# Performance work log

Hardware: AMD Instinct MI355X
Metric: run time of the kernel (lower is better)

## Reference

```python
import jax, jax.numpy as jnp
import numpy as np

N_USER = 100000
N_ITEM = 50000
N = N_USER + N_ITEM  # 150000 nodes
D = 64               # embedding_size
L = 3                # num_layers
E = 2000000          # edges
B = 8192             # batch of (user, item_p, item_n) triples
INT_W, POP_W, TIDE_W = 0.1, 0.1, 0.2


def setup_inputs() -> dict:
    key = jax.random.key(0)
    ks = jax.random.split(key, 10)
    stdv = 1.0 / np.sqrt(D)
    emb_int = jax.random.uniform(ks[0], (N, D), minval=-stdv, maxval=stdv, dtype=jnp.float32)
    emb_pop = jax.random.uniform(ks[1], (N, D), minval=-stdv, maxval=stdv, dtype=jnp.float32)
    q = jax.random.uniform(ks[2], (N_ITEM,), dtype=jnp.float32)
    b = jax.random.uniform(ks[3], (N_ITEM,), dtype=jnp.float32)
    user = jax.random.randint(ks[4], (B, 1), 0, N_USER)
    item_p = jax.random.randint(ks[5], (B, 1), 0, N_ITEM)
    item_n = jax.random.randint(ks[6], (B, 1), 0, N_ITEM)
    mask = jax.random.randint(ks[7], (B, 1), 0, 2).astype(bool)
    edge_src = jax.random.randint(ks[8], (E,), 0, N)
    edge_dst = jax.random.randint(ks[9], (E,), 0, N)
    return {"emb_int": emb_int, "emb_pop": emb_pop, "q": q, "b": b,
            "user": user, "item_p": item_p, "item_n": item_n, "mask": mask,
            "edge_src": edge_src, "edge_dst": edge_dst}


def reference(emb_int, emb_pop, q, b, user, item_p, item_n, mask, edge_src, edge_dst):
    # --- LightGCN symmetric normalization coefficients (per edge) ---
    ones = jnp.ones(edge_src.shape, emb_int.dtype)
    deg_out = jax.ops.segment_sum(ones, edge_src, num_segments=N)
    deg_in = jax.ops.segment_sum(ones, edge_dst, num_segments=N)
    norm = (jax.lax.rsqrt(jnp.maximum(deg_out, 1.0))[edge_src]
            * jax.lax.rsqrt(jnp.maximum(deg_in, 1.0))[edge_dst])  # [E]

    def propagate(e0):
        # L layers of LGConv (gather-scale-scatter), mean over layer outputs incl. layer 0.
        # Dropout is identity in eval mode (training=False).
        acc, h = e0, e0
        for _ in range(L):
            h = jax.ops.segment_sum(h[edge_src] * norm[:, None], edge_dst, num_segments=N)
            acc = acc + h
        return acc / (L + 1)

    f_int = propagate(emb_int)  # [N, D]
    f_pop = propagate(emb_pop)  # [N, D]

    ip = item_p + N_USER  # item node ids
    inn = item_n + N_USER
    u_i, u_p = f_int[user], f_pop[user]          # [B, 1, D]
    pi_i, pi_p = f_int[ip], f_pop[ip]
    ni_i, ni_p = f_int[inn], f_pop[inn]

    p_score_int = jnp.sum(u_i * pi_i, axis=2)    # [B, 1]
    n_score_int = jnp.sum(u_i * ni_i, axis=2)
    p_score_pop = jnp.sum(u_p * pi_p, axis=2)
    n_score_pop = jnp.sum(u_p * ni_p, axis=2)
    p_score_total = p_score_int + p_score_pop
    n_score_total = n_score_int + n_score_pop

    mf = mask.astype(p_score_int.dtype)
    nmf = (~mask).astype(p_score_int.dtype)

    def mask_bpr(p, n, m):
        return -jnp.mean(m * jax.nn.log_sigmoid(p - n))

    def bpr(p, n):
        return -jnp.mean(jax.nn.log_sigmoid(p - n))

    loss_int = mask_bpr(p_score_int, n_score_int, mf)
    loss_pop = mask_bpr(n_score_pop, p_score_pop, mf) - mask_bpr(p_score_pop, n_score_pop, nmf)

    pop_p = jax.nn.softplus(q[item_p]) + jax.nn.softplus(b[item_p])  # [B, 1]
    pop_n = jax.nn.softplus(q[item_n]) + jax.nn.softplus(b[item_n])
    loss_tide = bpr(jnp.tanh(pop_p) * p_score_total, jnp.tanh(pop_n) * n_score_total)

    return INT_W * loss_int + POP_W * loss_pop + TIDE_W * loss_tide
```

## Files before the change

### kernel.cpp

```cpp
#include <hip/hip_runtime.h>
#include <hip/hip_bf16.h>
#include <math.h>

#define N_USER 100000
#define N_ITEM 50000
#define NNODE  150000
#define DIM    64
#define NEDGE  2000000
#define BSZ    8192
#define NTGT   (3*BSZ)
#define CB     586
#define NB     512
#define CH     ((NEDGE + NB - 1)/NB)
#define LBLK   2048
#define PREPB  (NNODE*32/256)
#define CAP    5120

typedef float v2f __attribute__((ext_vector_type(2)));

__device__ __forceinline__ float logsigf(float x){
    return fminf(x, 0.f) - log1pf(expf(-fabsf(x)));
}
__device__ __forceinline__ float softplusf(float x){
    return fmaxf(x, 0.f) + log1pf(expf(-fabsf(x)));
}
__device__ __forceinline__ v2f fp8x2_to_f32(unsigned short u){
    return __builtin_amdgcn_cvt_pk_f32_fp8((int)u, false);
}
__device__ __forceinline__ unsigned short f32_to_fp8x2(float a, float b){
    return (unsigned short)__builtin_amdgcn_cvt_pk_fp8_f32(a, b, 0, false);
}
__device__ __forceinline__ unsigned rfl(unsigned v){
    return (unsigned)__builtin_amdgcn_readfirstlane((int)v);
}

__device__ __forceinline__ void scanCB(unsigned* arr, unsigned* tmp){
    int t = threadIdx.x;
    int base = 3*t;
    unsigned a0=0,a1=0,a2=0;
    if(base   < CB) a0 = arr[base];
    if(base+1 < CB) a1 = arr[base+1];
    if(base+2 < CB) a2 = arr[base+2];
    unsigned s = a0+a1+a2;
    tmp[t]=s; __syncthreads();
    for(int off=1; off<256; off<<=1){
        unsigned v = (t>=off)? tmp[t-off] : 0u;
        __syncthreads();
        tmp[t] += v;
        __syncthreads();
    }
    unsigned excl = tmp[t]-s;
    if(base   < CB) arr[base]   = excl;
    if(base+1 < CB) arr[base+1] = excl+a0;
    if(base+2 < CB) arr[base+2] = excl+a0+a1;
    __syncthreads();
}

__global__ __launch_bounds__(256) void k_hist(const int* __restrict__ src, const int* __restrict__ dst,
                       unsigned* __restrict__ histD, unsigned* __restrict__ histS,
                       const float2* __restrict__ ei, const float2* __restrict__ ep,
                       unsigned* __restrict__ hC32,
                       const unsigned char* __restrict__ mask8, unsigned* __restrict__ mflag){
    if(blockIdx.x >= NB){
        if(blockIdx.x == NB + PREPB){
            __shared__ int any;
            if(threadIdx.x==0) any=0;
            __syncthreads();
            for(int i=threadIdx.x;i<BSZ;i+=256){ if((i&3) && mask8[i]) any=1; }
            __syncthreads();
            if(threadIdx.x==0) *mflag = (any!=0) ? 1u : 0u;
            return;
        }
        int idx = (blockIdx.x - NB)*256 + threadIdx.x;
        int n = idx>>5, c = idx&31;
        float2 va, vb;
        if(c<16){ va = ei[(size_t)n*32 + 2*c]; vb = ei[(size_t)n*32 + 2*c+1]; }
        else    { va = ep[(size_t)n*32 + 2*c-32]; vb = ep[(size_t)n*32 + 2*c-31]; }
        int d = __builtin_amdgcn_cvt_pk_fp8_f32(va.x, va.y, 0, false);
        d = __builtin_amdgcn_cvt_pk_fp8_f32(vb.x, vb.y, d, true);
        hC32[(size_t)n*32 + c] = (unsigned)d;
        return;
    }
    __shared__ unsigned hD[CB], hS[CB];
    for(int i=threadIdx.x;i<CB;i+=256){ hD[i]=0; hS[i]=0; }
    __syncthreads();
    int lo = blockIdx.x*CH, hi = min(lo+CH, NEDGE);
    for(int e=lo+threadIdx.x; e<hi; e+=256){
        atomicAdd(&hS[src[e]>>8],1u);
        atomicAdd(&hD[dst[e]>>8],1u);
    }
    __syncthreads();
    for(int i=threadIdx.x;i<CB;i+=256){
        histD[(size_t)i*NB + blockIdx.x]=hD[i];
        histS[(size_t)i*NB + blockIdx.x]=hS[i];
    }
}

__global__ __launch_bounds__(512) void k_colscan(unsigned* __restrict__ histD, unsigned* __restrict__ histS,
                          unsigned* __restrict__ ctD, unsigned* __restrict__ ctS){
    unsigned* hist = blockIdx.y ? histS : histD;
    unsigned* ct   = blockIdx.y ? ctS   : ctD;
    int b = blockIdx.x;
    __shared__ unsigned sh[512];
    unsigned v = hist[(size_t)b*NB + threadIdx.x];
    sh[threadIdx.x] = v;
    __syncthreads();
    for(int off=1; off<512; off<<=1){
        unsigned t = (threadIdx.x>=off)? sh[threadIdx.x-off] : 0u;
        __syncthreads();
        sh[threadIdx.x] += t;
        __syncthreads();
    }
    hist[(size_t)b*NB + threadIdx.x] = sh[threadIdx.x] - v;
    if(threadIdx.x==511) ct[b] = sh[511];
}

__global__ __launch_bounds__(1024) void k_bstart(const unsigned* __restrict__ ctD, const unsigned* __restrict__ ctS,
                         unsigned* __restrict__ bsD, unsigned* __restrict__ bsS){
    __shared__ unsigned sh[1024];
    unsigned v = (threadIdx.x<CB)? ctD[threadIdx.x] : 0u;
    sh[threadIdx.x]=v; __syncthreads();
    for(int off=1; off<1024; off<<=1){ unsigned t=(threadIdx.x>=off)?sh[threadIdx.x-off]:0u; __syncthreads(); sh[threadIdx.x]+=t; __syncthreads(); }
    if(threadIdx.x<CB) bsD[threadIdx.x]=sh[threadIdx.x]-v;
    if(threadIdx.x==CB-1) bsD[CB]=sh[threadIdx.x];
    __syncthreads();
    unsigned v2 = (threadIdx.x<CB)? ctS[threadIdx.x] : 0u;
    sh[threadIdx.x]=v2; __syncthreads();
    for(int off=1; off<1024; off<<=1){ unsigned t=(threadIdx.x>=off)?sh[threadIdx.x-off]:0u; __syncthreads(); sh[threadIdx.x]+=t; __syncthreads(); }
    if(threadIdx.x<CB) bsS[threadIdx.x]=sh[threadIdx.x]-v2;
    if(threadIdx.x==CB-1) bsS[CB]=sh[threadIdx.x];
}

__global__ __launch_bounds__(256) void k_scatter(const int* __restrict__ src, const int* __restrict__ dst,
                          const unsigned* __restrict__ histD, const unsigned* __restrict__ histS,
                          const unsigned* __restrict__ bsD, const unsigned* __restrict__ bsS,
                          unsigned* __restrict__ part, unsigned char* __restrict__ spart){
    __shared__ unsigned curD[CB], curS[CB];
    __shared__ unsigned lhD[CB], lhS[CB];
    __shared__ unsigned startD[CB], startS[CB];
    __shared__ unsigned tmp[256];
    __shared__ unsigned partl[CH];
    __shared__ unsigned short keyD[CH];
    __shared__ unsigned short keyS[CH];
    __shared__ unsigned char sl[CH];
    for(int i=threadIdx.x;i<CB;i+=256){
        curD[i]=bsD[i]+histD[(size_t)i*NB+blockIdx.x];
        curS[i]=bsS[i]+histS[(size_t)i*NB+blockIdx.x];
        lhD[i]=0; lhS[i]=0;
    }
    __syncthreads();
    int lo=blockIdx.x*CH, hi=min(lo+CH,NEDGE);
    int n = hi-lo;
    for(int e=lo+threadIdx.x;e<hi;e+=256){
        atomicAdd(&lhD[dst[e]>>8],1u);
        atomicAdd(&lhS[src[e]>>8],1u);
    }
    __syncthreads();
    scanCB(lhD, tmp);
    scanCB(lhS, tmp);
    for(int i=threadIdx.x;i<CB;i+=256){ startD[i]=lhD[i]; startS[i]=lhS[i]; }
    __syncthreads();
    for(int e=lo+threadIdx.x;e<hi;e+=256){
        int s=src[e], d=dst[e];
        unsigned bd=(unsigned)(d>>8);
        unsigned slot=atomicAdd(&lhD[bd],1u);
        partl[slot]=((unsigned)(d&255)<<18)|(unsigned)s;
        keyD[slot]=(unsigned short)bd;
        unsigned bs=(unsigned)(s>>8);
        unsigned sslot=atomicAdd(&lhS[bs],1u);
        sl[sslot]=(unsigned char)(s&255);
        keyS[sslot]=(unsigned short)bs;
    }
    __syncthreads();
    for(int k=threadIdx.x;k<n;k+=256){
        unsigned b=keyD[k];
        part[curD[b] + (unsigned)k - startD[b]] = partl[k];
    }
    for(int k=threadIdx.x;k<n;k+=256){
        unsigned b=keyS[k];
        spart[curS[b] + (unsigned)k - startS[b]] = sl[k];
    }
}

__global__ __launch_bounds__(256) void k_degO(const unsigned char* __restrict__ spart, const unsigned* __restrict__ bsS,
                       float* __restrict__ rsqO){
    __shared__ unsigned cnt[256];
    cnt[threadIdx.x]=0;
    __syncthreads();
    unsigned lo=bsS[blockIdx.x], hi=bsS[blockIdx.x+1];
    for(unsigned e=lo+threadIdx.x;e<hi;e+=256) atomicAdd(&cnt[spart[e]],1u);
    __syncthreads();
    int node=(blockIdx.x<<8)+(int)threadIdx.x;
    if(node<NNODE) rsqO[node]=rsqrtf(fmaxf((float)cnt[threadIdx.x],1.f));
}

__global__ __launch_bounds__(256) void k_csr(const unsigned* __restrict__ part, const unsigned* __restrict__ bsD,
                      const float* __restrict__ rsqO,
                      unsigned* __restrict__ rs, unsigned* __restrict__ degI,
                      unsigned* __restrict__ ec){
    __shared__ unsigned cnt[256], cur[256], sh[256];
    __shared__ float rsq[256];
    __shared__ unsigned partl[CAP];
    cnt[threadIdx.x]=0;
    __syncthreads();
    unsigned lo=bsD[blockIdx.x], hi=bsD[blockIdx.x+1];
    unsigned n = hi-lo;
    for(unsigned e=lo+threadIdx.x;e<hi;e+=256) atomicAdd(&cnt[part[e]>>18],1u);
    __syncthreads();
    unsigned c=cnt[threadIdx.x];
    sh[threadIdx.x]=c; __syncthreads();
    for(int o=1;o<256;o<<=1){ unsigned t=(threadIdx.x>=o)?sh[threadIdx.x-o]:0u; __syncthreads(); sh[threadIdx.x]+=t; __syncthreads(); }
    unsigned ex = sh[threadIdx.x]-c;
    rsq[threadIdx.x]=rsqrtf(fmaxf((float)c,1.f));
    cur[threadIdx.x]=ex;
    int node=(blockIdx.x<<8)+(int)threadIdx.x;
    if(node<NNODE){ degI[node]=c; rs[node]=lo+ex; }
    __syncthreads();
    if(n <= CAP){
        for(unsigned e=lo+threadIdx.x;e<hi;e+=256){
            unsigned p=part[e];
            unsigned slot=atomicAdd(&cur[p>>18],1u);
            partl[slot]=p;
        }
        __syncthreads();
        for(unsigned k=threadIdx.x;k<n;k+=256){
            unsigned p=partl[k];
            unsigned fb=p>>18, s=p&0x3FFFFu;
            float w=rsq[fb]*rsqO[s];
            unsigned w14=(unsigned)(w*16383.f + 0.5f);
            ec[lo+k]=(w14<<18)|s;
        }
    } else {
        for(unsigned e=lo+threadIdx.x;e<hi;e+=256){
            unsigned p=part[e];
            unsigned fb=p>>18, s=p&0x3FFFFu;
            unsigned pos=lo+atomicAdd(&cur[fb],1u);
            float w=rsq[fb]*rsqO[s];
            unsigned w14=(unsigned)(w*16383.f + 0.5f);
            ec[pos]=(w14<<18)|s;
        }
    }
}

__device__ __forceinline__ void drain_row(const unsigned short* __restrict__ hin,
                                          const unsigned* __restrict__ ec,
                                          unsigned s, unsigned c, unsigned &i, int lane,
                                          float &ax, float &ay){
    for(; i+4<=c; i+=4){
        unsigned e0=ec[s+i], e1=ec[s+i+1], e2=ec[s+i+2], e3=ec[s+i+3];
        unsigned short u0=hin[(size_t)(e0&0x3FFFFu)*64+lane];
        unsigned short u1=hin[(size_t)(e1&0x3FFFFu)*64+lane];
        unsigned short u2=hin[(size_t)(e2&0x3FFFFu)*64+lane];
        unsigned short u3=hin[(size_t)(e3&0x3FFFFu)*64+lane];
        float w0=(float)(e0>>18)*(1.f/16383.f), w1=(float)(e1>>18)*(1.f/16383.f);
        float w2=(float)(e2>>18)*(1.f/16383.f), w3=(float)(e3>>18)*(1.f/16383.f);
        v2f v;
        v=fp8x2_to_f32(u0); ax+=w0*v.x; ay+=w0*v.y;
        v=fp8x2_to_f32(u1); ax+=w1*v.x; ay+=w1*v.y;
        v=fp8x2_to_f32(u2); ax+=w2*v.x; ay+=w2*v.y;
        v=fp8x2_to_f32(u3); ax+=w3*v.x; ay+=w3*v.y;
    }
    for(; i<c; ++i){
        unsigned e0=ec[s+i];
        unsigned short u0=hin[(size_t)(e0&0x3FFFFu)*64+lane];
        float w0=(float)(e0>>18)*(1.f/16383.f);
        v2f v=fp8x2_to_f32(u0); ax+=w0*v.x; ay+=w0*v.y;
    }
}

__global__ __launch_bounds__(256) void k_spmm_c(const unsigned short* __restrict__ hin, unsigned short* __restrict__ hout,
                                                const unsigned* __restrict__ rs, const unsigned* __restrict__ degI,
                                                const unsigned* __restrict__ ec){
    int wv = (blockIdx.x*256 + threadIdx.x) >> 6;
    int lane = threadIdx.x & 63;
    int r = 4*wv;
    if(r >= NNODE) return;
    unsigned s0=rfl(rs[r  ]), c0=rfl(degI[r  ]);
    unsigned s1=rfl(rs[r+1]), c1=rfl(degI[r+1]);
    unsigned s2=rfl(rs[r+2]), c2=rfl(degI[r+2]);
    unsigned s3=rfl(rs[r+3]), c3=rfl(degI[r+3]);
    float ax0=0,ay0=0, ax1=0,ay1=0, ax2=0,ay2=0, ax3=0,ay3=0;
    unsigned i0=0,i1=0,i2=0,i3=0;
    while(i0+4<=c0 && i1+4<=c1 && i2+4<=c2 && i3+4<=c3){
        unsigned e00=ec[s0+i0], e01=ec[s0+i0+1], e02=ec[s0+i0+2], e03=ec[s0+i0+3];
        unsigned e10=ec[s1+i1], e11=ec[s1+i1+1], e12=ec[s1+i1+2], e13=ec[s1+i1+3];
        unsigned e20=ec[s2+i2], e21=ec[s2+i2+1], e22=ec[s2+i2+2], e23=ec[s2+i2+3];
        unsigned e30=ec[s3+i3], e31=ec[s3+i3+1], e32=ec[s3+i3+2], e33=ec[s3+i3+3];
        unsigned short u00=hin[(size_t)(e00&0x3FFFFu)*64+lane];
        unsigned short u01=hin[(size_t)(e01&0x3FFFFu)*64+lane];
        unsigned short u02=hin[(size_t)(e02&0x3FFFFu)*64+lane];
        unsigned short u03=hin[(size_t)(e03&0x3FFFFu)*64+lane];
        unsigned short u10=hin[(size_t)(e10&0x3FFFFu)*64+lane];
        unsigned short u11=hin[(size_t)(e11&0x3FFFFu)*64+lane];
        unsigned short u12=hin[(size_t)(e12&0x3FFFFu)*64+lane];
        unsigned short u13=hin[(size_t)(e13&0x3FFFFu)*64+lane];
        unsigned short u20=hin[(size_t)(e20&0x3FFFFu)*64+lane];
        unsigned short u21=hin[(size_t)(e21&0x3FFFFu)*64+lane];
        unsigned short u22=hin[(size_t)(e22&0x3FFFFu)*64+lane];
        unsigned short u23=hin[(size_t)(e23&0x3FFFFu)*64+lane];
        unsigned short u30=hin[(size_t)(e30&0x3FFFFu)*64+lane];
        unsigned short u31=hin[(size_t)(e31&0x3FFFFu)*64+lane];
        unsigned short u32v=hin[(size_t)(e32&0x3FFFFu)*64+lane];
        unsigned short u33=hin[(size_t)(e33&0x3FFFFu)*64+lane];
        v2f v;
        v=fp8x2_to_f32(u00); ax0+=(float)(e00>>18)*(1.f/16383.f)*v.x; ay0+=(float)(e00>>18)*(1.f/16383.f)*v.y;
        v=fp8x2_to_f32(u01); ax0+=(float)(e01>>18)*(1.f/16383.f)*v.x; ay0+=(float)(e01>>18)*(1.f/16383.f)*v.y;
        v=fp8x2_to_f32(u02); ax0+=(float)(e02>>18)*(1.f/16383.f)*v.x; ay0+=(float)(e02>>18)*(1.f/16383.f)*v.y;
        v=fp8x2_to_f32(u03); ax0+=(float)(e03>>18)*(1.f/16383.f)*v.x; ay0+=(float)(e03>>18)*(1.f/16383.f)*v.y;
        v=fp8x2_to_f32(u10); ax1+=(float)(e10>>18)*(1.f/16383.f)*v.x; ay1+=(float)(e10>>18)*(1.f/16383.f)*v.y;
        v=fp8x2_to_f32(u11); ax1+=(float)(e11>>18)*(1.f/16383.f)*v.x; ay1+=(float)(e11>>18)*(1.f/16383.f)*v.y;
        v=fp8x2_to_f32(u12); ax1+=(float)(e12>>18)*(1.f/16383.f)*v.x; ay1+=(float)(e12>>18)*(1.f/16383.f)*v.y;
        v=fp8x2_to_f32(u13); ax1+=(float)(e13>>18)*(1.f/16383.f)*v.x; ay1+=(float)(e13>>18)*(1.f/16383.f)*v.y;
        v=fp8x2_to_f32(u20); ax2+=(float)(e20>>18)*(1.f/16383.f)*v.x; ay2+=(float)(e20>>18)*(1.f/16383.f)*v.y;
        v=fp8x2_to_f32(u21); ax2+=(float)(e21>>18)*(1.f/16383.f)*v.x; ay2+=(float)(e21>>18)*(1.f/16383.f)*v.y;
        v=fp8x2_to_f32(u22); ax2+=(float)(e22>>18)*(1.f/16383.f)*v.x; ay2+=(float)(e22>>18)*(1.f/16383.f)*v.y;
        v=fp8x2_to_f32(u23); ax2+=(float)(e23>>18)*(1.f/16383.f)*v.x; ay2+=(float)(e23>>18)*(1.f/16383.f)*v.y;
        v=fp8x2_to_f32(u30); ax3+=(float)(e30>>18)*(1.f/16383.f)*v.x; ay3+=(float)(e30>>18)*(1.f/16383.f)*v.y;
        v=fp8x2_to_f32(u31); ax3+=(float)(e31>>18)*(1.f/16383.f)*v.x; ay3+=(float)(e31>>18)*(1.f/16383.f)*v.y;
        v=fp8x2_to_f32(u32v); ax3+=(float)(e32>>18)*(1.f/16383.f)*v.x; ay3+=(float)(e32>>18)*(1.f/16383.f)*v.y;
        v=fp8x2_to_f32(u33); ax3+=(float)(e33>>18)*(1.f/16383.f)*v.x; ay3+=(float)(e33>>18)*(1.f/16383.f)*v.y;
        i0+=4; i1+=4; i2+=4; i3+=4;
    }
    drain_row(hin, ec, s0, c0, i0, lane, ax0, ay0);
    drain_row(hin, ec, s1, c1, i1, lane, ax1, ay1);
    drain_row(hin, ec, s2, c2, i2, lane, ax2, ay2);
    drain_row(hin, ec, s3, c3, i3, lane, ax3, ay3);
    hout[(size_t)(r  )*64+lane] = f32_to_fp8x2(ax0, ay0);
    hout[(size_t)(r+1)*64+lane] = f32_to_fp8x2(ax1, ay1);
    hout[(size_t)(r+2)*64+lane] = f32_to_fp8x2(ax2, ay2);
    hout[(size_t)(r+3)*64+lane] = f32_to_fp8x2(ax3, ay3);
}

__global__ __launch_bounds__(256) void k_spmm_t(const unsigned short* __restrict__ hin, float2* __restrict__ h3,
                                                const unsigned* __restrict__ rs, const unsigned* __restrict__ degI,
                                                const unsigned* __restrict__ ec,
                                                const int* __restrict__ user, const int* __restrict__ itp,
                                                const int* __restrict__ itn){
    int wv = (blockIdx.x*256 + threadIdx.x) >> 6;
    int lane = threadIdx.x & 63;
    int t0 = 2*wv, t1 = 2*wv+1;
    if(t0 >= NTGT) return;
    int sec0 = t0>>13, b0 = t0&(BSZ-1);
    int sec1 = t1>>13, b1 = t1&(BSZ-1);
    int n0 = (sec0==0) ? user[b0] : ((sec0==1) ? itp[b0]+N_USER : itn[b0]+N_USER);
    int n1 = (sec1==0) ? user[b1] : ((sec1==1) ? itp[b1]+N_USER : itn[b1]+N_USER);
    n0 = __builtin_amdgcn_readfirstlane(n0);
    n1 = __builtin_amdgcn_readfirstlane(n1);
    unsigned s0 = rfl(rs[n0]), c0 = rfl(degI[n0]);
    unsigned s1 = rfl(rs[n1]), c1 = rfl(degI[n1]);
    float ax0=0.f, ay0=0.f, ax1=0.f, ay1=0.f;
    unsigned i0=0, i1=0;
    while(i0+4<=c0 && i1+4<=c1){
        unsigned e0=ec[s0+i0], e1=ec[s0+i0+1], e2=ec[s0+i0+2], e3=ec[s0+i0+3];
        unsigned e4=ec[s1+i1], e5=ec[s1+i1+1], e6=ec[s1+i1+2], e7=ec[s1+i1+3];
        unsigned short u0=hin[(size_t)(e0&0x3FFFFu)*64+lane];
        unsigned short u1=hin[(size_t)(e1&0x3FFFFu)*64+lane];
        unsigned short u2=hin[(size_t)(e2&0x3FFFFu)*64+lane];
        unsigned short u3=hin[(size_t)(e3&0x3FFFFu)*64+lane];
        unsigned short u4=hin[(size_t)(e4&0x3FFFFu)*64+lane];
        unsigned short u5=hin[(size_t)(e5&0x3FFFFu)*64+lane];
        unsigned short u6=hin[(size_t)(e6&0x3FFFFu)*64+lane];
        unsigned short u7=hin[(size_t)(e7&0x3FFFFu)*64+lane];
        float w0=(float)(e0>>18)*(1.f/16383.f), w1=(float)(e1>>18)*(1.f/16383.f);
        float w2=(float)(e2>>18)*(1.f/16383.f), w3=(float)(e3>>18)*(1.f/16383.f);
        float w4=(float)(e4>>18)*(1.f/16383.f), w5=(float)(e5>>18)*(1.f/16383.f);
        float w6=(float)(e6>>18)*(1.f/16383.f), w7=(float)(e7>>18)*(1.f/16383.f);
        v2f v;
        v=fp8x2_to_f32(u0); ax0+=w0*v.x; ay0+=w0*v.y;
        v=fp8x2_to_f32(u1); ax0+=w1*v.x; ay0+=w1*v.y;
        v=fp8x2_to_f32(u2); ax0+=w2*v.x; ay0+=w2*v.y;
        v=fp8x2_to_f32(u3); ax0+=w3*v.x; ay0+=w3*v.y;
        v=fp8x2_to_f32(u4); ax1+=w4*v.x; ay1+=w4*v.y;
        v=fp8x2_to_f32(u5); ax1+=w5*v.x; ay1+=w5*v.y;
        v=fp8x2_to_f32(u6); ax1+=w6*v.x; ay1+=w6*v.y;
        v=fp8x2_to_f32(u7); ax1+=w7*v.x; ay1+=w7*v.y;
        i0+=4; i1+=4;
    }
    drain_row(hin, ec, s0, c0, i0, lane, ax0, ay0);
    drain_row(hin, ec, s1, c1, i1, lane, ax1, ay1);
    h3[(size_t)t0*64+lane] = make_float2(ax0, ay0);
    h3[(size_t)t1*64+lane] = make_float2(ax1, ay1);
}

__global__ __launch_bounds__(256) void k_scoreloss(const float2* __restrict__ ei, const float2* __restrict__ ep,
                        const unsigned short* __restrict__ h1C, const unsigned short* __restrict__ h2C,
                        const float2* __restrict__ h3,
                        const float* __restrict__ q, const float* __restrict__ bq,
                        const int* __restrict__ user, const int* __restrict__ item_p, const int* __restrict__ item_n,
                        const void* __restrict__ mask, const unsigned* __restrict__ mflag,
                        float4* __restrict__ partial){
    int t = blockIdx.x*256 + threadIdx.x;
    int b = t >> 6, l = t & 63;
    int wv = threadIdx.x >> 6;
    __shared__ float4 wsum[4];
    int nu = user[b];
    int np = item_p[b] + N_USER;
    int nn = item_n[b] + N_USER;

    float2 e0u, e0p, e0n;
    if(l < 32){
        e0u = ei[(size_t)nu*32 + l]; e0p = ei[(size_t)np*32 + l]; e0n = ei[(size_t)nn*32 + l];
    } else {
        e0u = ep[(size_t)nu*32 + (l-32)]; e0p = ep[(size_t)np*32 + (l-32)]; e0n = ep[(size_t)nn*32 + (l-32)];
    }
    v2f h1u = fp8x2_to_f32(h1C[(size_t)nu*64 + l]);
    v2f h1p = fp8x2_to_f32(h1C[(size_t)np*64 + l]);
    v2f h1n = fp8x2_to_f32(h1C[(size_t)nn*64 + l]);
    v2f h2u = fp8x2_to_f32(h2C[(size_t)nu*64 + l]);
    v2f h2p = fp8x2_to_f32(h2C[(size_t)np*64 + l]);
    v2f h2n = fp8x2_to_f32(h2C[(size_t)nn*64 + l]);
    float2 h3u = h3[(size_t)b*64 + l];
    float2 h3p = h3[(size_t)(BSZ   + b)*64 + l];
    float2 h3n = h3[(size_t)(2*BSZ + b)*64 + l];

    float fux = e0u.x + h1u.x + h2u.x + h3u.x, fuy = e0u.y + h1u.y + h2u.y + h3u.y;
    float fpx = e0p.x + h1p.x + h2p.x + h3p.x, fpy = e0p.y + h1p.y + h2p.y + h3p.y;
    float fnx = e0n.x + h1n.x + h2n.x + h3n.x, fny = e0n.y + h1n.y + h2n.y + h3n.y;

    float dp = fux*fpx + fuy*fpy;
    float dn = fux*fnx + fuy*fny;
    for(int off=16; off; off>>=1){ dp += __shfl_down(dp,off,32); dn += __shfl_down(dn,off,32); }
    float pi  = __shfl(dp, 0, 64) * (1.f/16.f);
    float ni  = __shfl(dn, 0, 64) * (1.f/16.f);
    float pp  = __shfl(dp, 32, 64) * (1.f/16.f);
    float npp = __shfl(dn, 32, 64) * (1.f/16.f);
    if(l == 0){
        bool bytes = (*mflag)!=0;
        float mf = bytes ? (((const unsigned char*)mask)[b]?1.f:0.f)
                         : (((const int*)mask)[b]?1.f:0.f);
        float nmf = 1.f-mf;
        float a0 = mf  * logsigf(pi-ni);
        float a1 = mf  * logsigf(npp-pp);
        float a2 = nmf * logsigf(pp-npp);
        int ip=item_p[b], in_=item_n[b];
        float popp = softplusf(q[ip]) + softplusf(bq[ip]);
        float popn = softplusf(q[in_]) + softplusf(bq[in_]);
        float a3 = logsigf(tanhf(popp)*(pi+pp) - tanhf(popn)*(ni+npp));
        wsum[wv] = make_float4(a0,a1,a2,a3);
    }
    __syncthreads();
    if(threadIdx.x == 0){
        float4 s0=wsum[0], s1=wsum[1], s2=wsum[2], s3=wsum[3];
        partial[blockIdx.x] = make_float4(s0.x+s1.x+s2.x+s3.x, s0.y+s1.y+s2.y+s3.y,
                                          s0.z+s1.z+s2.z+s3.z, s0.w+s1.w+s2.w+s3.w);
    }
}

__global__ __launch_bounds__(256) void k_lossfin(const float4* __restrict__ partial, float* __restrict__ out){
    __shared__ float4 sh[256];
    float4 s = make_float4(0,0,0,0);
    for(int i=threadIdx.x; i<LBLK; i+=256){
        float4 v = partial[i];
        s.x+=v.x; s.y+=v.y; s.z+=v.z; s.w+=v.w;
    }
    sh[threadIdx.x]=s;
    __syncthreads();
    for(int off=128; off; off>>=1){
        if(threadIdx.x < off){
            float4 a=sh[threadIdx.x], b2=sh[threadIdx.x+off];
            sh[threadIdx.x]=make_float4(a.x+b2.x,a.y+b2.y,a.z+b2.z,a.w+b2.w);
        }
        __syncthreads();
    }
    if(threadIdx.x==0){
        const float invB = 1.f/(float)BSZ;
        float4 t = sh[0];
        float loss_int  = -t.x*invB;
        float loss_pop  = -t.y*invB + t.z*invB;
        float loss_tide = -t.w*invB;
        out[0] = 0.1f*loss_int + 0.1f*loss_pop + 0.2f*loss_tide;
    }
}

extern "C" void kernel_launch(void* const* d_in, const int* in_sizes, int n_in,
                              void* d_out, int out_size, void* d_ws, size_t ws_size,
                              hipStream_t stream){
    const float* emb_int = (const float*)d_in[0];
    const float* emb_pop = (const float*)d_in[1];
    const float* q    = (const float*)d_in[2];
    const float* bq   = (const float*)d_in[3];
    const int* user   = (const int*)d_in[4];
    const int* item_p = (const int*)d_in[5];
    const int* item_n = (const int*)d_in[6];
    const void* mask  = d_in[7];
    const int* esrc   = (const int*)d_in[8];
    const int* edst   = (const int*)d_in[9];

    char* ws = (char*)d_ws;
    size_t o = 0;
    auto take = [&](size_t bytes)->char*{ char* p = ws + o; o = (o + bytes + 255) & ~(size_t)255; return p; };
    unsigned* histD = (unsigned*)take((size_t)CB*NB*4);
    unsigned* histS = (unsigned*)take((size_t)CB*NB*4);
    unsigned* ctD   = (unsigned*)take((size_t)CB*4);
    unsigned* ctS   = (unsigned*)take((size_t)CB*4);
    unsigned* bsD   = (unsigned*)take((size_t)(CB+1)*4);
    unsigned* bsS   = (unsigned*)take((size_t)(CB+1)*4);
    unsigned* part  = (unsigned*)take((size_t)NEDGE*4);
    unsigned char* spart = (unsigned char*)take((size_t)NEDGE);
    float*    rsqO  = (float*)take((size_t)NNODE*4);
    unsigned* degI  = (unsigned*)take((size_t)NNODE*4);
    unsigned* rs    = (unsigned*)take((size_t)NNODE*4);
    unsigned* ec    = (unsigned*)take((size_t)NEDGE*4);
    unsigned short* hE  = (unsigned short*)take((size_t)NNODE*64*2);
    unsigned short* h1C = (unsigned short*)take((size_t)NNODE*64*2);
    unsigned short* h2C = (unsigned short*)take((size_t)NNODE*64*2);
    float2*   h3    = (float2*)take((size_t)NTGT*64*8);
    float4*   partial = (float4*)take((size_t)LBLK*16);
    unsigned* mflag = (unsigned*)take(256);
    (void)ws_size; (void)in_sizes; (void)n_in; (void)out_size;

    k_hist<<<NB + PREPB + 1,256,0,stream>>>(esrc, edst, histD, histS,
                                            (const float2*)emb_int, (const float2*)emb_pop,
                                            (unsigned*)hE, (const unsigned char*)mask, mflag);
    k_colscan<<<dim3(CB,2),512,0,stream>>>(histD, histS, ctD, ctS);
    k_bstart<<<1,1024,0,stream>>>(ctD, ctS, bsD, bsS);
    k_scatter<<<NB,256,0,stream>>>(esrc, edst, histD, histS, bsD, bsS, part, spart);
    k_degO<<<CB,256,0,stream>>>(spart, bsS, rsqO);
    k_csr<<<CB,256,0,stream>>>(part, bsD, rsqO, rs, degI, ec);

    const int spB = ((NNODE/4)*64 + 255)/256;
    k_spmm_c<<<spB,256,0,stream>>>(hE,  h1C, rs, degI, ec);
    k_spmm_c<<<spB,256,0,stream>>>(h1C, h2C, rs, degI, ec);
    k_spmm_t<<<((NTGT/2)*64 + 255)/256,256,0,stream>>>(h2C, h3, rs, degI, ec,
                                                 user, item_p, item_n);
    k_scoreloss<<<LBLK,256,0,stream>>>((const float2*)emb_int, (const float2*)emb_pop,
                                       h1C, h2C, h3, q, bq, user, item_p, item_n,
                                       mask, mflag, partial);
    k_lossfin<<<1,256,0,stream>>>(partial, (float*)d_out);
}
```

Before: 352.5 us.

## Sort rows by in-degree for balanced SpMM waves; transpose histogram layout

Adds a degree histogram and a counting-sort kernel that orders nodes by in-degree. The SpMM kernel processes rows in that order, so the four rows handled by one wave have similar lengths and the shared unrolled loop wastes fewer iterations. The per-block histograms are also stored block-major so the histogram and scatter kernels access contiguous memory, while the column scan now reads with a stride. This costs an extra kernel launch, an indirection per row, and scattered output rows.

```diff
diff --git a/kernel.cpp b/kernel.cpp
--- a/kernel.cpp
+++ b/kernel.cpp
@@ -15,6 +15,7 @@
 #define LBLK   2048
 #define PREPB  (NNODE*32/256)
 #define CAP    5120
+#define DB     128
 
 typedef float v2f __attribute__((ext_vector_type(2)));
 
@@ -60,11 +61,13 @@
                        unsigned* __restrict__ histD, unsigned* __restrict__ histS,
                        const float2* __restrict__ ei, const float2* __restrict__ ep,
                        unsigned* __restrict__ hC32,
-                       const unsigned char* __restrict__ mask8, unsigned* __restrict__ mflag){
+                       const unsigned char* __restrict__ mask8, unsigned* __restrict__ mflag,
+                       unsigned* __restrict__ dhist, unsigned* __restrict__ dcur){
     if(blockIdx.x >= NB){
         if(blockIdx.x == NB + PREPB){
             __shared__ int any;
             if(threadIdx.x==0) any=0;
+            if(threadIdx.x < DB){ dhist[threadIdx.x]=0u; dcur[threadIdx.x]=0u; }
             __syncthreads();
             for(int i=threadIdx.x;i<BSZ;i+=256){ if((i&3) && mask8[i]) any=1; }
             __syncthreads();
@@ -91,8 +94,8 @@
     }
     __syncthreads();
     for(int i=threadIdx.x;i<CB;i+=256){
-        histD[(size_t)i*NB + blockIdx.x]=hD[i];
-        histS[(size_t)i*NB + blockIdx.x]=hS[i];
+        histD[(size_t)blockIdx.x*CB + i]=hD[i];
+        histS[(size_t)blockIdx.x*CB + i]=hS[i];
     }
 }
 
@@ -102,7 +105,7 @@
     unsigned* ct   = blockIdx.y ? ctS   : ctD;
     int b = blockIdx.x;
     __shared__ unsigned sh[512];
-    unsigned v = hist[(size_t)b*NB + threadIdx.x];
+    unsigned v = hist[(size_t)threadIdx.x*CB + b];
     sh[threadIdx.x] = v;
     __syncthreads();
     for(int off=1; off<512; off<<=1){
@@ -111,7 +114,7 @@
         sh[threadIdx.x] += t;
         __syncthreads();
     }
-    hist[(size_t)b*NB + threadIdx.x] = sh[threadIdx.x] - v;
+    hist[(size_t)threadIdx.x*CB + b] = sh[threadIdx.x] - v;
     if(threadIdx.x==511) ct[b] = sh[511];
 }
 
@@ -144,8 +147,8 @@
     __shared__ unsigned short keyS[CH];
     __shared__ unsigned char sl[CH];
     for(int i=threadIdx.x;i<CB;i+=256){
-        curD[i]=bsD[i]+histD[(size_t)i*NB+blockIdx.x];
-        curS[i]=bsS[i]+histS[(size_t)i*NB+blockIdx.x];
+        curD[i]=bsD[i]+histD[(size_t)blockIdx.x*CB+i];
+        curS[i]=bsS[i]+histS[(size_t)blockIdx.x*CB+i];
         lhD[i]=0; lhS[i]=0;
     }
     __syncthreads();
@@ -197,11 +200,12 @@
 __global__ __launch_bounds__(256) void k_csr(const unsigned* __restrict__ part, const unsigned* __restrict__ bsD,
                       const float* __restrict__ rsqO,
                       unsigned* __restrict__ rs, unsigned* __restrict__ degI,
-                      unsigned* __restrict__ ec){
-    __shared__ unsigned cnt[256], cur[256], sh[256];
+                      unsigned* __restrict__ ec, unsigned* __restrict__ dhist){
+    __shared__ unsigned cnt[256], cur[256], sh[256], ldh[DB];
     __shared__ float rsq[256];
     __shared__ unsigned partl[CAP];
     cnt[threadIdx.x]=0;
+    if(threadIdx.x<DB) ldh[threadIdx.x]=0;
     __syncthreads();
     unsigned lo=bsD[blockIdx.x], hi=bsD[blockIdx.x+1];
     unsigned n = hi-lo;
@@ -214,8 +218,12 @@
     rsq[threadIdx.x]=rsqrtf(fmaxf((float)c,1.f));
     cur[threadIdx.x]=ex;
     int node=(blockIdx.x<<8)+(int)threadIdx.x;
-    if(node<NNODE){ degI[node]=c; rs[node]=lo+ex; }
-    __syncthreads();
+    if(node<NNODE){
+        degI[node]=c; rs[node]=lo+ex;
+        atomicAdd(&ldh[min(c,(unsigned)(DB-1))],1u);
+    }
+    __syncthreads();
+    if(threadIdx.x<DB && ldh[threadIdx.x]) atomicAdd(&dhist[threadIdx.x], ldh[threadIdx.x]);
     if(n <= CAP){
         for(unsigned e=lo+threadIdx.x;e<hi;e+=256){
             unsigned p=part[e];
@@ -242,6 +250,22 @@
     }
 }
 
+__global__ __launch_bounds__(256) void k_dorder(const unsigned* __restrict__ degI,
+                        const unsigned* __restrict__ dhist, unsigned* __restrict__ dcur,
+                        unsigned* __restrict__ ord){
+    __shared__ unsigned dbase[DB], lh[DB], claim[DB];
+    if(threadIdx.x==0){ unsigned run=0; for(int i=0;i<DB;i++){ dbase[i]=run; run+=dhist[i]; } }
+    if(threadIdx.x<DB) lh[threadIdx.x]=0;
+    __syncthreads();
+    int node = blockIdx.x*256 + threadIdx.x;
+    unsigned myb=0, myrank=0; bool valid = node<NNODE;
+    if(valid){ myb = min(degI[node],(unsigned)(DB-1)); myrank = atomicAdd(&lh[myb],1u); }
+    __syncthreads();
+    if(threadIdx.x<DB && lh[threadIdx.x]) claim[threadIdx.x] = atomicAdd(&dcur[threadIdx.x], lh[threadIdx.x]);
+    __syncthreads();
+    if(valid) ord[dbase[myb] + claim[myb] + myrank] = (unsigned)node;
+}
+
 __device__ __forceinline__ void drain_row(const unsigned short* __restrict__ hin,
                                           const unsigned* __restrict__ ec,
                                           unsigned s, unsigned c, unsigned &i, int lane,
@@ -270,15 +294,16 @@
 
 __global__ __launch_bounds__(256) void k_spmm_c(const unsigned short* __restrict__ hin, unsigned short* __restrict__ hout,
                                                 const unsigned* __restrict__ rs, const unsigned* __restrict__ degI,
-                                                const unsigned* __restrict__ ec){
+                                                const unsigned* __restrict__ ec, const unsigned* __restrict__ ord){
     int wv = (blockIdx.x*256 + threadIdx.x) >> 6;
     int lane = threadIdx.x & 63;
-    int r = 4*wv;
-    if(r >= NNODE) return;
-    unsigned s0=rfl(rs[r  ]), c0=rfl(degI[r  ]);
-    unsigned s1=rfl(rs[r+1]), c1=rfl(degI[r+1]);
-    unsigned s2=rfl(rs[r+2]), c2=rfl(degI[r+2]);
-    unsigned s3=rfl(rs[r+3]), c3=rfl(degI[r+3]);
+    if(4*wv >= NNODE) return;
+    unsigned r0=rfl(ord[4*wv  ]), r1=rfl(ord[4*wv+1]);
+    unsigned r2=rfl(ord[4*wv+2]), r3=rfl(ord[4*wv+3]);
+    unsigned s0=rfl(rs[r0]), c0=rfl(degI[r0]);
+    unsigned s1=rfl(rs[r1]), c1=rfl(degI[r1]);
+    unsigned s2=rfl(rs[r2]), c2=rfl(degI[r2]);
+    unsigned s3=rfl(rs[r3]), c3=rfl(degI[r3]);
     float ax0=0,ay0=0, ax1=0,ay1=0, ax2=0,ay2=0, ax3=0,ay3=0;
     unsigned i0=0,i1=0,i2=0,i3=0;
     while(i0+4<=c0 && i1+4<=c1 && i2+4<=c2 && i3+4<=c3){
@@ -302,33 +327,33 @@
         unsigned short u31=hin[(size_t)(e31&0x3FFFFu)*64+lane];
         unsigned short u32v=hin[(size_t)(e32&0x3FFFFu)*64+lane];
         unsigned short u33=hin[(size_t)(e33&0x3FFFFu)*64+lane];
-        v2f v;
-        v=fp8x2_to_f32(u00); ax0+=(float)(e00>>18)*(1.f/16383.f)*v.x; ay0+=(float)(e00>>18)*(1.f/16383.f)*v.y;
-        v=fp8x2_to_f32(u01); ax0+=(float)(e01>>18)*(1.f/16383.f)*v.x; ay0+=(float)(e01>>18)*(1.f/16383.f)*v.y;
-        v=fp8x2_to_f32(u02); ax0+=(float)(e02>>18)*(1.f/16383.f)*v.x; ay0+=(float)(e02>>18)*(1.f/16383.f)*v.y;
-        v=fp8x2_to_f32(u03); ax0+=(float)(e03>>18)*(1.f/16383.f)*v.x; ay0+=(float)(e03>>18)*(1.f/16383.f)*v.y;
-        v=fp8x2_to_f32(u10); ax1+=(float)(e10>>18)*(1.f/16383.f)*v.x; ay1+=(float)(e10>>18)*(1.f/16383.f)*v.y;
-        v=fp8x2_to_f32(u11); ax1+=(float)(e11>>18)*(1.f/16383.f)*v.x; ay1+=(float)(e11>>18)*(1.f/16383.f)*v.y;
-        v=fp8x2_to_f32(u12); ax1+=(float)(e12>>18)*(1.f/16383.f)*v.x; ay1+=(float)(e12>>18)*(1.f/16383.f)*v.y;
-        v=fp8x2_to_f32(u13); ax1+=(float)(e13>>18)*(1.f/16383.f)*v.x; ay1+=(float)(e13>>18)*(1.f/16383.f)*v.y;
-        v=fp8x2_to_f32(u20); ax2+=(float)(e20>>18)*(1.f/16383.f)*v.x; ay2+=(float)(e20>>18)*(1.f/16383.f)*v.y;
-        v=fp8x2_to_f32(u21); ax2+=(float)(e21>>18)*(1.f/16383.f)*v.x; ay2+=(float)(e21>>18)*(1.f/16383.f)*v.y;
-        v=fp8x2_to_f32(u22); ax2+=(float)(e22>>18)*(1.f/16383.f)*v.x; ay2+=(float)(e22>>18)*(1.f/16383.f)*v.y;
-        v=fp8x2_to_f32(u23); ax2+=(float)(e23>>18)*(1.f/16383.f)*v.x; ay2+=(float)(e23>>18)*(1.f/16383.f)*v.y;
-        v=fp8x2_to_f32(u30); ax3+=(float)(e30>>18)*(1.f/16383.f)*v.x; ay3+=(float)(e30>>18)*(1.f/16383.f)*v.y;
-        v=fp8x2_to_f32(u31); ax3+=(float)(e31>>18)*(1.f/16383.f)*v.x; ay3+=(float)(e31>>18)*(1.f/16383.f)*v.y;
-        v=fp8x2_to_f32(u32v); ax3+=(float)(e32>>18)*(1.f/16383.f)*v.x; ay3+=(float)(e32>>18)*(1.f/16383.f)*v.y;
-        v=fp8x2_to_f32(u33); ax3+=(float)(e33>>18)*(1.f/16383.f)*v.x; ay3+=(float)(e33>>18)*(1.f/16383.f)*v.y;
+        v2f v; float w;
+        v=fp8x2_to_f32(u00); w=(float)(e00>>18)*(1.f/16383.f); ax0+=w*v.x; ay0+=w*v.y;
+        v=fp8x2_to_f32(u01); w=(float)(e01>>18)*(1.f/16383.f); ax0+=w*v.x; ay0+=w*v.y;
+        v=fp8x2_to_f32(u02); w=(float)(e02>>18)*(1.f/16383.f); ax0+=w*v.x; ay0+=w*v.y;
+        v=fp8x2_to_f32(u03); w=(float)(e03>>18)*(1.f/16383.f); ax0+=w*v.x; ay0+=w*v.y;
+        v=fp8x2_to_f32(u10); w=(float)(e10>>18)*(1.f/16383.f); ax1+=w*v.x; ay1+=w*v.y;
+        v=fp8x2_to_f32(u11); w=(float)(e11>>18)*(1.f/16383.f); ax1+=w*v.x; ay1+=w*v.y;
+        v=fp8x2_to_f32(u12); w=(float)(e12>>18)*(1.f/16383.f); ax1+=w*v.x; ay1+=w*v.y;
+        v=fp8x2_to_f32(u13); w=(float)(e13>>18)*(1.f/16383.f); ax1+=w*v.x; ay1+=w*v.y;
+        v=fp8x2_to_f32(u20); w=(float)(e20>>18)*(1.f/16383.f); ax2+=w*v.x; ay2+=w*v.y;
+        v=fp8x2_to_f32(u21); w=(float)(e21>>18)*(1.f/16383.f); ax2+=w*v.x; ay2+=w*v.y;
+        v=fp8x2_to_f32(u22); w=(float)(e22>>18)*(1.f/16383.f); ax2+=w*v.x; ay2+=w*v.y;
+        v=fp8x2_to_f32(u23); w=(float)(e23>>18)*(1.f/16383.f); ax2+=w*v.x; ay2+=w*v.y;
+        v=fp8x2_to_f32(u30); w=(float)(e30>>18)*(1.f/16383.f); ax3+=w*v.x; ay3+=w*v.y;
+        v=fp8x2_to_f32(u31); w=(float)(e31>>18)*(1.f/16383.f); ax3+=w*v.x; ay3+=w*v.y;
+        v=fp8x2_to_f32(u32v); w=(float)(e32>>18)*(1.f/16383.f); ax3+=w*v.x; ay3+=w*v.y;
+        v=fp8x2_to_f32(u33); w=(float)(e33>>18)*(1.f/16383.f); ax3+=w*v.x; ay3+=w*v.y;
         i0+=4; i1+=4; i2+=4; i3+=4;
     }
     drain_row(hin, ec, s0, c0, i0, lane, ax0, ay0);
     drain_row(hin, ec, s1, c1, i1, lane, ax1, ay1);
     drain_row(hin, ec, s2, c2, i2, lane, ax2, ay2);
     drain_row(hin, ec, s3, c3, i3, lane, ax3, ay3);
-    hout[(size_t)(r  )*64+lane] = f32_to_fp8x2(ax0, ay0);
-    hout[(size_t)(r+1)*64+lane] = f32_to_fp8x2(ax1, ay1);
-    hout[(size_t)(r+2)*64+lane] = f32_to_fp8x2(ax2, ay2);
-    hout[(size_t)(r+3)*64+lane] = f32_to_fp8x2(ax3, ay3);
+    hout[(size_t)r0*64+lane] = f32_to_fp8x2(ax0, ay0);
+    hout[(size_t)r1*64+lane] = f32_to_fp8x2(ax1, ay1);
+    hout[(size_t)r2*64+lane] = f32_to_fp8x2(ax2, ay2);
+    hout[(size_t)r3*64+lane] = f32_to_fp8x2(ax3, ay3);
 }
 
 __global__ __launch_bounds__(256) void k_spmm_t(const unsigned short* __restrict__ hin, float2* __restrict__ h3,
@@ -489,8 +514,8 @@
     char* ws = (char*)d_ws;
     size_t o = 0;
     auto take = [&](size_t bytes)->char*{ char* p = ws + o; o = (o + bytes + 255) & ~(size_t)255; return p; };
-    unsigned* histD = (unsigned*)take((size_t)CB*NB*4);
-    unsigned* histS = (unsigned*)take((size_t)CB*NB*4);
+    unsigned* histD = (unsigned*)take((size_t)NB*CB*4);
+    unsigned* histS = (unsigned*)take((size_t)NB*CB*4);
     unsigned* ctD   = (unsigned*)take((size_t)CB*4);
     unsigned* ctS   = (unsigned*)take((size_t)CB*4);
     unsigned* bsD   = (unsigned*)take((size_t)(CB+1)*4);
@@ -507,20 +532,25 @@
     float2*   h3    = (float2*)take((size_t)NTGT*64*8);
     float4*   partial = (float4*)take((size_t)LBLK*16);
     unsigned* mflag = (unsigned*)take(256);
+    unsigned* dhist = (unsigned*)take((size_t)DB*4);
+    unsigned* dcur  = (unsigned*)take((size_t)DB*4);
+    unsigned* ord   = (unsigned*)take((size_t)NNODE*4);
     (void)ws_size; (void)in_sizes; (void)n_in; (void)out_size;
 
     k_hist<<<NB + PREPB + 1,256,0,stream>>>(esrc, edst, histD, histS,
                                             (const float2*)emb_int, (const float2*)emb_pop,
-                                            (unsigned*)hE, (const unsigned char*)mask, mflag);
+                                            (unsigned*)hE, (const unsigned char*)mask, mflag,
+                                            dhist, dcur);
     k_colscan<<<dim3(CB,2),512,0,stream>>>(histD, histS, ctD, ctS);
     k_bstart<<<1,1024,0,stream>>>(ctD, ctS, bsD, bsS);
     k_scatter<<<NB,256,0,stream>>>(esrc, edst, histD, histS, bsD, bsS, part, spart);
     k_degO<<<CB,256,0,stream>>>(spart, bsS, rsqO);
-    k_csr<<<CB,256,0,stream>>>(part, bsD, rsqO, rs, degI, ec);
+    k_csr<<<CB,256,0,stream>>>(part, bsD, rsqO, rs, degI, ec, dhist);
+    k_dorder<<<CB,256,0,stream>>>(degI, dhist, dcur, ord);
 
     const int spB = ((NNODE/4)*64 + 255)/256;
-    k_spmm_c<<<spB,256,0,stream>>>(hE,  h1C, rs, degI, ec);
-    k_spmm_c<<<spB,256,0,stream>>>(h1C, h2C, rs, degI, ec);
+    k_spmm_c<<<spB,256,0,stream>>>(hE,  h1C, rs, degI, ec, ord);
+    k_spmm_c<<<spB,256,0,stream>>>(h1C, h2C, rs, degI, ec, ord);
     k_spmm_t<<<((NTGT/2)*64 + 255)/256,256,0,stream>>>(h2C, h3, rs, degI, ec,
                                                  user, item_p, item_n);
     k_scoreloss<<<LBLK,256,0,stream>>>((const float2*)emb_int, (const float2*)emb_pop,
```

After: 369.2 us. 4.7% more time.
